# Kernel optimization log

Hardware: AMD Instinct MI355X
Metric: run time of the kernel (lower is better)

The kernel has to match this reference:

```python
import jax, jax.numpy as jnp
import numpy as np

B, DIN, DH, DOUT = 256, 784, 512, 10


def _softplus(x):
    # matches torch.log(1.0 + torch.exp(x)) exactly
    return jnp.log(1.0 + jnp.exp(x))


def _kl(w_mu, w_sigma_sp, size_in):
    # compute_kl_loss(w_mu, diag_embed(softplus(w_sigma))) without materializing diag
    # w_mu: (in, out), w_sigma_sp: (out, in)
    trace = jnp.sum(w_sigma_sp, axis=1)            # (out,)
    mu_sq = jnp.sum(w_mu * w_mu, axis=0)           # (out,)
    logdet = jnp.sum(jnp.log(w_sigma_sp), axis=1)  # slogdet of diag = sum log diag
    return 0.5 * jnp.sum(trace + mu_sq - size_in - logdet)


def setup_inputs() -> dict:
    key = jax.random.key(0)
    ks = jax.random.split(key, 9)
    inp = {
        "x": jax.random.normal(ks[0], (B, DIN, 1), dtype=jnp.float32),
        "w_mu1": 5e-5 * jax.random.normal(ks[1], (DIN, DH), dtype=jnp.float32),
        "w_sigma1": jax.random.uniform(ks[2], (DH, DIN), minval=-12.0, maxval=-2.0, dtype=jnp.float32),
        "b_mu1": 5e-5 * jax.random.normal(ks[3], (DH, 1), dtype=jnp.float32),
        "b_sigma1": jax.random.uniform(ks[4], (DH,), minval=-12.0, maxval=-2.0, dtype=jnp.float32),
        "w_mu2": 5e-5 * jax.random.normal(ks[5], (DH, DOUT), dtype=jnp.float32),
        "w_sigma2": jax.random.uniform(ks[6], (DOUT, DH), minval=-12.0, maxval=-2.0, dtype=jnp.float32),
        "b_mu2": 5e-5 * jax.random.normal(ks[7], (DOUT, 1), dtype=jnp.float32),
        "b_sigma2": jax.random.uniform(ks[8], (DOUT,), minval=-12.0, maxval=-2.0, dtype=jnp.float32),
    }
    return inp


def reference(x, w_mu1, w_sigma1, b_mu1, b_sigma1, w_mu2, w_sigma2, b_mu2, b_sigma2):
    batch = x.shape[0]
    eye_h = jnp.eye(DH, dtype=x.dtype)
    eye_o = jnp.eye(DOUT, dtype=x.dtype)

    # ---- RVLinearlayer 1 (sigma_in = None) ----
    xv = x[..., 0]                                   # (B, DIN)
    mu1 = jnp.einsum('io,bi->bo', w_mu1, xv)[:, :, None] + b_mu1   # (B, DH, 1)
    Ws1 = _softplus(w_sigma1)                        # (DH, DIN)
    quad1 = jnp.einsum('hi,bi->bh', Ws1, xv * xv)    # mu_in^T diag(Ws) mu_in per unit
    sigma1 = quad1[:, :, None] * eye_h + jnp.diag(_softplus(b_sigma1))  # (B, DH, DH)
    kl1 = _kl(w_mu1, Ws1, DIN)

    # ---- RVNonLinearFunc (ReLU) ----
    mu2 = jax.nn.relu(mu1)                           # (B, DH, 1)
    g = (mu1[..., 0] > 0).astype(x.dtype)            # Heaviside grad of relu
    sigma2 = sigma1 * (g[:, :, None] * g[:, None, :])

    # ---- RVLinearlayer 2 (with sigma_in) ----
    m2v = mu2[..., 0]                                # (B, DH)
    mu3 = jnp.einsum('ho,bh->bo', w_mu2, m2v)[:, :, None] + b_mu2   # (B, DOUT, 1)
    Ws2 = _softplus(w_sigma2)                        # (DOUT, DH)
    quad2 = jnp.einsum('oh,bh->bo', Ws2, m2v * m2v)  # (B, DOUT)
    # faithful replication of W_Sigma.view(out,-1) @ sigma_in.view(-1,B) then .view(B,out)
    Sflat = sigma2.reshape(DH * DH, batch)           # same row-major view as torch
    diag_rows = Sflat[jnp.arange(DH) * (DH + 1)]     # rows of the diag positions, (DH, B)
    tr = (Ws2 @ diag_rows).reshape(batch, DOUT)      # (out,B) -> row-major (B,out)
    mid = jnp.einsum('ho,bhk,kp->bop', w_mu2, sigma2, w_mu2)  # w_mu2^T Sigma w_mu2
    sigma3 = (tr[:, :, None] * eye_o + mid + quad2[:, :, None] * eye_o
              + jnp.diag(_softplus(b_sigma2)))       # (B, DOUT, DOUT)
    kl2 = _kl(w_mu2, Ws2, DH)

    # ---- RVSoftmax ----
    p = jax.nn.softmax(mu3[..., 0], axis=1)          # (B, DOUT)
    jac = p[:, :, None] * eye_o - p[:, :, None] * p[:, None, :]  # diag(p) - p p^T
    Sigma_out = jnp.einsum('bij,bjk,blk->bil', jac, sigma3, jac)

    return p, Sigma_out, kl1 + kl2
```

## Files before the change

### kernel.cpp

```cpp
#include <hip/hip_runtime.h>
#include <math.h>

#define BATCH 256
#define DIN 784
#define DH 512
#define DOUT 10
#define SPLITS 16
#define KSPL 49

__device__ __forceinline__ float softplus(float x) {
  return __logf(1.0f + __expf(x));
}

__global__ __launch_bounds__(256) void gemm1_kernel(
    const float* __restrict__ x, const float* __restrict__ w_mu1,
    const float* __restrict__ w_sigma1, const float* __restrict__ w_mu2,
    const float* __restrict__ w_sigma2, float* __restrict__ mu_part,
    float* __restrict__ q_part, float* __restrict__ kl_part) {
  __shared__ float xs[16][KSPL];
  __shared__ float wmt[KSPL][66];
  __shared__ float wst[KSPL][66];
  __shared__ float rlds[4];
  const int t = threadIdx.x;
  const int h0 = blockIdx.x * 64;
  const int b0 = blockIdx.y * 16;
  const int s = blockIdx.z;
  const int i0 = s * KSPL;
  const int hl = (t & 31) * 2;
  const int bl = t >> 5;

  for (int f = t; f < 16 * KSPL; f += 256) {
    const int bb = f / KSPL, kk = f - bb * KSPL;
    xs[bb][kk] = x[(b0 + bb) * DIN + i0 + kk];
  }
  for (int f = t; f < KSPL * 64; f += 256) {
    const int kk = f >> 6, hh = f & 63;
    wmt[kk][hh] = w_mu1[(i0 + kk) * DH + h0 + hh];
  }
  for (int f = t; f < 64 * KSPL; f += 256) {
    const int hh = f / KSPL, kk = f - hh * KSPL;
    wst[kk][hh] = softplus(w_sigma1[(h0 + hh) * DIN + i0 + kk]);
  }
  __syncthreads();

  float mu00 = 0.f, mu10 = 0.f, mu01 = 0.f, mu11 = 0.f;
  float q00 = 0.f, q10 = 0.f, q01 = 0.f, q11 = 0.f;

#pragma unroll 7
  for (int kk = 0; kk < KSPL; kk++) {
    const float2 wmv = *(const float2*)&wmt[kk][hl];
    const float2 wsv = *(const float2*)&wst[kk][hl];
    const float xa = xs[bl][kk];
    const float xb = xs[bl + 8][kk];
    const float xa2 = xa * xa;
    const float xb2 = xb * xb;
    mu00 = fmaf(wmv.x, xa, mu00);
    mu10 = fmaf(wmv.y, xa, mu10);
    mu01 = fmaf(wmv.x, xb, mu01);
    mu11 = fmaf(wmv.y, xb, mu11);
    q00 = fmaf(wsv.x, xa2, q00);
    q10 = fmaf(wsv.y, xa2, q10);
    q01 = fmaf(wsv.x, xb2, q01);
    q11 = fmaf(wsv.y, xb2, q11);
  }

  const int h = h0 + hl;
  const int bA = b0 + bl, bB = b0 + bl + 8;
  const size_t base = (size_t)s * (BATCH * DH);
  *(float2*)&mu_part[base + (size_t)bA * DH + h] = make_float2(mu00, mu10);
  *(float2*)&mu_part[base + (size_t)bB * DH + h] = make_float2(mu01, mu11);
  *(float2*)&q_part[base + (size_t)bA * DH + h] = make_float2(q00, q10);
  *(float2*)&q_part[base + (size_t)bB * DH + h] = make_float2(q01, q11);

  float kl = 0.f;
  int slot = -1;
  if (blockIdx.y == 0) {
    for (int f = t; f < KSPL * 64; f += 256) {
      const int kk = f >> 6, hh = f & 63;
      const float sv = wst[kk][hh];
      kl += sv - __logf(sv);
    }
    slot = blockIdx.x * 16 + s;
  } else if (blockIdx.y == 1) {
    for (int f = t; f < KSPL * 64; f += 256) {
      const int kk = f >> 6, hh = f & 63;
      const float wv = wmt[kk][hh];
      kl = fmaf(wv, wv, kl);
    }
    slot = 128 + blockIdx.x * 16 + s;
  } else if (blockIdx.y == 2 && blockIdx.x == 0) {
    for (int idx = s * 320 + t; idx < s * 320 + 320; idx += 256) {
      const float sv = softplus(w_sigma2[idx]);
      const float wv = w_mu2[idx];
      kl += sv - __logf(sv);
      kl = fmaf(wv, wv, kl);
    }
    slot = 256 + s;
  }

  for (int off = 32; off > 0; off >>= 1) kl += __shfl_down(kl, off);
  const int lane = t & 63, wv = t >> 6;
  if (lane == 0) rlds[wv] = kl;
  __syncthreads();
  if (t == 0 && slot >= 0)
    kl_part[slot] = rlds[0] + rlds[1] + rlds[2] + rlds[3];
}

__global__ __launch_bounds__(256) void layer2_kernel(
    const float* __restrict__ mu_part, const float* __restrict__ q_part,
    const float* __restrict__ b_mu1, const float* __restrict__ b_sigma1,
    const float* __restrict__ w_mu2, const float* __restrict__ w_sigma2,
    const float* __restrict__ b_mu2, const float* __restrict__ b_sigma2,
    const float* __restrict__ kl_part, float* __restrict__ out_p,
    float* __restrict__ out_sigma, float* __restrict__ out_kl) {
  const int b = blockIdx.x, t = threadIdx.x;
  __shared__ float red[4][75];
  __shared__ float fin[75];
  __shared__ float mu3[10], pvec[10], trv[10], spb2[10];
  __shared__ float sig[10][10], Tm[10][10], cs[10], rs[10];
  __shared__ float klred[4];

  float musum0 = 0.f, musum1 = 0.f, qsum0 = 0.f, qsum1 = 0.f;
#pragma unroll
  for (int s2 = 0; s2 < SPLITS; s2++) {
    const size_t base = (size_t)s2 * (BATCH * DH) + (size_t)b * DH;
    musum0 += mu_part[base + t];
    musum1 += mu_part[base + t + 256];
    qsum0 += q_part[base + t];
    qsum1 += q_part[base + t + 256];
  }

  float m2v[2], d2v[2];
  {
    const float ma0 = musum0 + b_mu1[t];
    const float ma1 = musum1 + b_mu1[t + 256];
    m2v[0] = ma0 > 0.f ? ma0 : 0.f;
    m2v[1] = ma1 > 0.f ? ma1 : 0.f;
    d2v[0] = ma0 > 0.f ? (qsum0 + softplus(b_sigma1[t])) : 0.f;
    d2v[1] = ma1 > 0.f ? (qsum1 + softplus(b_sigma1[t + 256])) : 0.f;
  }

  float acc[75];
#pragma unroll
  for (int i = 0; i < 75; i++) acc[i] = 0.f;

#pragma unroll
  for (int hh = 0; hh < 2; hh++) {
    const int h = t + hh * 256;
    const float m2h = m2v[hh], d2h = d2v[hh];
    const float msq = m2h * m2h;
    float wrow[10];
#pragma unroll
    for (int o = 0; o < 10; o++) wrow[o] = w_mu2[h * 10 + o];
#pragma unroll
    for (int o = 0; o < 10; o++) {
      acc[o] = fmaf(wrow[o], m2h, acc[o]);
      acc[10 + o] = fmaf(softplus(w_sigma2[o * DH + h]), msq, acc[10 + o]);
    }
    int idx = 20;
#pragma unroll
    for (int o = 0; o < 10; o++) {
      const float wd = wrow[o] * d2h;
#pragma unroll
      for (int p = o; p < 10; p++) {
        acc[idx] = fmaf(wd, wrow[p], acc[idx]);
        idx++;
      }
    }
  }

  const int lane = t & 63, wv = t >> 6;
#pragma unroll
  for (int j = 0; j < 75; j++) {
    float v = acc[j];
    for (int off = 32; off > 0; off >>= 1) v += __shfl_down(v, off);
    if (lane == 0) red[wv][j] = v;
  }
  __syncthreads();
  if (t < 75) fin[t] = red[0][t] + red[1][t] + red[2][t] + red[3][t];
  __syncthreads();

  if (t < 10) {
    mu3[t] = fin[t] + b_mu2[t];
    spb2[t] = softplus(b_sigma2[t]);
    const int c0 = b * 10 + t;
    const int o2 = c0 >> 8, cc = c0 & 255;
    float mua = b_mu1[cc], qa = 0.f;
    float mub = b_mu1[256 + cc], qb = 0.f;
#pragma unroll
    for (int s2 = 0; s2 < SPLITS; s2++) {
      const size_t base = (size_t)s2 * (BATCH * DH) + (size_t)cc * DH;
      mua += mu_part[base + cc];
      qa += q_part[base + cc];
      mub += mu_part[base + 256 + cc];
      qb += q_part[base + 256 + cc];
    }
    const float d2aa = mua > 0.f ? (qa + softplus(b_sigma1[cc])) : 0.f;
    const float d2bb = mub > 0.f ? (qb + softplus(b_sigma1[256 + cc])) : 0.f;
    trv[t] = softplus(w_sigma2[o2 * DH + 2 * cc]) * d2aa +
             softplus(w_sigma2[o2 * DH + 2 * cc + 1]) * d2bb;
  }
  __syncthreads();

  if (t == 0) {
    float mx = mu3[0];
#pragma unroll
    for (int o = 1; o < 10; o++) mx = fmaxf(mx, mu3[o]);
    float e[10], se = 0.f;
#pragma unroll
    for (int o = 0; o < 10; o++) {
      e[o] = expf(mu3[o] - mx);
      se += e[o];
    }
    const float inv = 1.f / se;
#pragma unroll
    for (int o = 0; o < 10; o++) pvec[o] = e[o] * inv;
  }
  __syncthreads();

  if (t < 100) {
    const int o = t / 10, p = t % 10;
    const int i0 = o < p ? o : p, j0 = o < p ? p : o;
    const int idx = 10 * i0 - (i0 * (i0 - 1)) / 2 + (j0 - i0);
    float v = fin[20 + idx];
    if (o == p) v += trv[o] + fin[10 + o] + spb2[o];
    sig[o][p] = v;
  }
  __syncthreads();

  if (t < 10) {
    float s = 0.f;
#pragma unroll
    for (int j = 0; j < 10; j++) s = fmaf(pvec[j], sig[j][t], s);
    cs[t] = s;
  }
  __syncthreads();

  if (t < 100) {
    const int o = t / 10, p = t % 10;
    Tm[o][p] = pvec[o] * (sig[o][p] - cs[p]);
  }
  __syncthreads();

  if (t < 10) {
    float s = 0.f;
#pragma unroll
    for (int k = 0; k < 10; k++) s = fmaf(Tm[t][k], pvec[k], s);
    rs[t] = s;
  }
  __syncthreads();

  if (t < 100) {
    const int o = t / 10, p = t % 10;
    out_sigma[b * 100 + t] = pvec[p] * (Tm[o][p] - rs[o]);
  }
  if (t < 10) out_p[b * 10 + t] = pvec[t];

  float klv = 0.f;
  if (b == 0) {
    klv = kl_part[t];
    if (t < 16) klv += kl_part[256 + t];
  }
  for (int off = 32; off > 0; off >>= 1) klv += __shfl_down(klv, off);
  if (lane == 0) klred[wv] = klv;
  __syncthreads();
  if (b == 0 && t == 0) {
    out_kl[0] =
        0.5f * (klred[0] + klred[1] + klred[2] + klred[3] - 406528.0f);
  }
}

extern "C" void kernel_launch(void* const* d_in, const int* in_sizes, int n_in,
                              void* d_out, int out_size, void* d_ws,
                              size_t ws_size, hipStream_t stream) {
  const float* x = (const float*)d_in[0];
  const float* w_mu1 = (const float*)d_in[1];
  const float* w_sigma1 = (const float*)d_in[2];
  const float* b_mu1 = (const float*)d_in[3];
  const float* b_sigma1 = (const float*)d_in[4];
  const float* w_mu2 = (const float*)d_in[5];
  const float* w_sigma2 = (const float*)d_in[6];
  const float* b_mu2 = (const float*)d_in[7];
  const float* b_sigma2 = (const float*)d_in[8];

  float* out = (float*)d_out;
  float* out_p = out;
  float* out_sigma = out + 2560;
  float* out_kl = out + 28160;

  float* ws = (float*)d_ws;
  float* mu_part = ws;
  float* q_part = ws + SPLITS * BATCH * DH;
  float* kl_part = ws + 2 * SPLITS * BATCH * DH;

  gemm1_kernel<<<dim3(8, 16, 16), 256, 0, stream>>>(
      x, w_mu1, w_sigma1, w_mu2, w_sigma2, mu_part, q_part, kl_part);
  layer2_kernel<<<256, 256, 0, stream>>>(mu_part, q_part, b_mu1, b_sigma1,
                                         w_mu2, w_sigma2, b_mu2, b_sigma2,
                                         kl_part, out_p, out_sigma, out_kl);
}
```

Baseline: 128.3 us.

## Enlarge gemm1 tiles to 64x64 with 4x4 register blocking, vectorize split reduction

The first-layer GEMM block tile grows from 16 batch rows to 64. Each thread now computes a 4x4 register tile from float4 weight loads and float2 x loads, with the K dimension padded from 49 to 50 so the inner loop can step by two. This cuts the grid from 2048 to 512 blocks, and the softplus of w_sigma1 is recomputed 4x fewer times across blocks. layer2 now reduces the split partials with float4 loads into shared memory. Per-thread register use and LDS use go up, and fewer blocks may lower occupancy. The kl branches keyed on blockIdx.y still seem to assume the old tiling, so they may be affected.

```diff
diff --git a/kernel.cpp b/kernel.cpp
--- a/kernel.cpp
+++ b/kernel.cpp
@@ -17,19 +17,19 @@
     const float* __restrict__ w_sigma1, const float* __restrict__ w_mu2,
     const float* __restrict__ w_sigma2, float* __restrict__ mu_part,
     float* __restrict__ q_part, float* __restrict__ kl_part) {
-  __shared__ float xs[16][KSPL];
-  __shared__ float wmt[KSPL][66];
-  __shared__ float wst[KSPL][66];
+  __shared__ float xs[64][50];
+  __shared__ float wmt[50][68];
+  __shared__ float wst[50][68];
   __shared__ float rlds[4];
   const int t = threadIdx.x;
   const int h0 = blockIdx.x * 64;
-  const int b0 = blockIdx.y * 16;
+  const int b0 = blockIdx.y * 64;
   const int s = blockIdx.z;
   const int i0 = s * KSPL;
-  const int hl = (t & 31) * 2;
-  const int bl = t >> 5;
-
-  for (int f = t; f < 16 * KSPL; f += 256) {
+  const int hl = (t & 15) * 4;
+  const int bg = (t >> 4) * 4;
+
+  for (int f = t; f < 64 * KSPL; f += 256) {
     const int bb = f / KSPL, kk = f - bb * KSPL;
     xs[bb][kk] = x[(b0 + bb) * DIN + i0 + kk];
   }
@@ -41,36 +41,55 @@
     const int hh = f / KSPL, kk = f - hh * KSPL;
     wst[kk][hh] = softplus(w_sigma1[(h0 + hh) * DIN + i0 + kk]);
   }
-  __syncthreads();
-
-  float mu00 = 0.f, mu10 = 0.f, mu01 = 0.f, mu11 = 0.f;
-  float q00 = 0.f, q10 = 0.f, q01 = 0.f, q11 = 0.f;
-
-#pragma unroll 7
-  for (int kk = 0; kk < KSPL; kk++) {
-    const float2 wmv = *(const float2*)&wmt[kk][hl];
-    const float2 wsv = *(const float2*)&wst[kk][hl];
-    const float xa = xs[bl][kk];
-    const float xb = xs[bl + 8][kk];
-    const float xa2 = xa * xa;
-    const float xb2 = xb * xb;
-    mu00 = fmaf(wmv.x, xa, mu00);
-    mu10 = fmaf(wmv.y, xa, mu10);
-    mu01 = fmaf(wmv.x, xb, mu01);
-    mu11 = fmaf(wmv.y, xb, mu11);
-    q00 = fmaf(wsv.x, xa2, q00);
-    q10 = fmaf(wsv.y, xa2, q10);
-    q01 = fmaf(wsv.x, xb2, q01);
-    q11 = fmaf(wsv.y, xb2, q11);
+  if (t < 64) {
+    xs[t][49] = 0.f;
+    wmt[49][t] = 0.f;
+    wst[49][t] = 0.f;
+  }
+  __syncthreads();
+
+  float mu[4][4], qq[4][4];
+#pragma unroll
+  for (int j = 0; j < 4; j++)
+#pragma unroll
+    for (int i = 0; i < 4; i++) {
+      mu[j][i] = 0.f;
+      qq[j][i] = 0.f;
+    }
+
+#pragma unroll 5
+  for (int kk = 0; kk < 50; kk += 2) {
+    const float4 wm0 = *(const float4*)&wmt[kk][hl];
+    const float4 wm1 = *(const float4*)&wmt[kk + 1][hl];
+    const float4 ws0 = *(const float4*)&wst[kk][hl];
+    const float4 ws1 = *(const float4*)&wst[kk + 1][hl];
+    const float* wm0a = (const float*)&wm0;
+    const float* wm1a = (const float*)&wm1;
+    const float* ws0a = (const float*)&ws0;
+    const float* ws1a = (const float*)&ws1;
+#pragma unroll
+    for (int j = 0; j < 4; j++) {
+      const float2 xv = *(const float2*)&xs[bg + j][kk];
+      const float xx = xv.x, xy = xv.y;
+      const float x2 = xx * xx, y2 = xy * xy;
+#pragma unroll
+      for (int i = 0; i < 4; i++) {
+        mu[j][i] = fmaf(wm0a[i], xx, mu[j][i]);
+        mu[j][i] = fmaf(wm1a[i], xy, mu[j][i]);
+        qq[j][i] = fmaf(ws0a[i], x2, qq[j][i]);
+        qq[j][i] = fmaf(ws1a[i], y2, qq[j][i]);
+      }
+    }
   }
 
   const int h = h0 + hl;
-  const int bA = b0 + bl, bB = b0 + bl + 8;
   const size_t base = (size_t)s * (BATCH * DH);
-  *(float2*)&mu_part[base + (size_t)bA * DH + h] = make_float2(mu00, mu10);
-  *(float2*)&mu_part[base + (size_t)bB * DH + h] = make_float2(mu01, mu11);
-  *(float2*)&q_part[base + (size_t)bA * DH + h] = make_float2(q00, q10);
-  *(float2*)&q_part[base + (size_t)bB * DH + h] = make_float2(q01, q11);
+#pragma unroll
+  for (int j = 0; j < 4; j++) {
+    const size_t row = base + (size_t)(b0 + bg + j) * DH + h;
+    *(float4*)&mu_part[row] = make_float4(mu[j][0], mu[j][1], mu[j][2], mu[j][3]);
+    *(float4*)&q_part[row] = make_float4(qq[j][0], qq[j][1], qq[j][2], qq[j][3]);
+  }
 
   float kl = 0.f;
   int slot = -1;
@@ -114,30 +133,40 @@
     const float* __restrict__ kl_part, float* __restrict__ out_p,
     float* __restrict__ out_sigma, float* __restrict__ out_kl) {
   const int b = blockIdx.x, t = threadIdx.x;
+  __shared__ float smu[DH], sq[DH];
   __shared__ float red[4][75];
   __shared__ float fin[75];
   __shared__ float mu3[10], pvec[10], trv[10], spb2[10];
   __shared__ float sig[10][10], Tm[10][10], cs[10], rs[10];
   __shared__ float klred[4];
 
-  float musum0 = 0.f, musum1 = 0.f, qsum0 = 0.f, qsum1 = 0.f;
-#pragma unroll
-  for (int s2 = 0; s2 < SPLITS; s2++) {
-    const size_t base = (size_t)s2 * (BATCH * DH) + (size_t)b * DH;
-    musum0 += mu_part[base + t];
-    musum1 += mu_part[base + t + 256];
-    qsum0 += q_part[base + t];
-    qsum1 += q_part[base + t + 256];
-  }
+  {
+    const int arr = t >> 7;
+    const int h4 = (t & 127) * 4;
+    const float* srcbase = (arr == 0 ? mu_part : q_part);
+    const float4* src = (const float4*)(srcbase + (size_t)b * DH + h4);
+    float4 a = make_float4(0.f, 0.f, 0.f, 0.f);
+#pragma unroll
+    for (int s2 = 0; s2 < SPLITS; s2++) {
+      const float4 v = src[(size_t)s2 * (BATCH * DH / 4)];
+      a.x += v.x;
+      a.y += v.y;
+      a.z += v.z;
+      a.w += v.w;
+    }
+    float* dst = (arr == 0 ? smu : sq);
+    *(float4*)&dst[h4] = a;
+  }
+  __syncthreads();
 
   float m2v[2], d2v[2];
   {
-    const float ma0 = musum0 + b_mu1[t];
-    const float ma1 = musum1 + b_mu1[t + 256];
+    const float ma0 = smu[t] + b_mu1[t];
+    const float ma1 = smu[t + 256] + b_mu1[t + 256];
     m2v[0] = ma0 > 0.f ? ma0 : 0.f;
     m2v[1] = ma1 > 0.f ? ma1 : 0.f;
-    d2v[0] = ma0 > 0.f ? (qsum0 + softplus(b_sigma1[t])) : 0.f;
-    d2v[1] = ma1 > 0.f ? (qsum1 + softplus(b_sigma1[t + 256])) : 0.f;
+    d2v[0] = ma0 > 0.f ? (sq[t] + softplus(b_sigma1[t])) : 0.f;
+    d2v[1] = ma1 > 0.f ? (sq[t + 256] + softplus(b_sigma1[t + 256])) : 0.f;
   }
 
   float acc[75];
@@ -293,7 +322,7 @@
   float* q_part = ws + SPLITS * BATCH * DH;
   float* kl_part = ws + 2 * SPLITS * BATCH * DH;
 
-  gemm1_kernel<<<dim3(8, 16, 16), 256, 0, stream>>>(
+  gemm1_kernel<<<dim3(8, 4, 16), 256, 0, stream>>>(
       x, w_mu1, w_sigma1, w_mu2, w_sigma2, mu_part, q_part, kl_part);
   layer2_kernel<<<256, 256, 0, stream>>>(mu_part, q_part, b_mu1, b_sigma1,
                                          w_mu2, w_sigma2, b_mu2, b_sigma2,
```

Measured after the change: 122.3 us. -4.7%, faster.
